# Optimization experiments

Hardware: AMD Instinct MI355X
Metric: run time of the kernel (lower is better)

## Reference

```python
import jax, jax.numpy as jnp
import numpy as np

CC = 0.25  # commitment cost
K1 = 4096
K2 = 4096
D1 = 64
D2 = 64

def conv1d(x, w, b, stride=1, pad=0):
    # x: [N,C,T], w: [O,I,K] (torch layout)
    y = jax.lax.conv_general_dilated(x, w, (stride,), [(pad, pad)],
                                     dimension_numbers=('NCH', 'OIH', 'NCH'))
    return y + b[None, :, None]

def convT1d(x, w, b, stride=2, pad=1):
    # torch ConvTranspose1d weight layout: [Cin, Cout, K]
    k = w.shape[-1]
    w2 = jnp.flip(w, -1).transpose(1, 0, 2)  # -> [Cout, Cin, K]
    y = jax.lax.conv_general_dilated(x, w2, (1,), [(k - 1 - pad, k - 1 - pad)],
                                     lhs_dilation=(stride,),
                                     dimension_numbers=('NCH', 'OIH', 'NCH'))
    return y + b[None, :, None]

def resblocks(x, w1, b1, w2, b2):
    # w1: [n, C, C, 3], w2: [n, C, C, 1]; n is small & fixed (2)
    for i in range(w1.shape[0]):
        h = conv1d(jax.nn.relu(x), w1[i], b1[i], 1, 1)
        h = conv1d(jax.nn.relu(h), w2[i], b2[i], 1, 0)
        x = x + h
    return x

def quantize(x, embed):
    # x: [B,D,T]; embed: [K,D]
    b, d, t = x.shape
    xf = x.transpose(0, 2, 1).reshape(-1, d)               # [N,D]
    dist = (xf * xf).sum(1, keepdims=True) - 2.0 * (xf @ embed.T) + (embed * embed).sum(1)
    idx = jnp.argmin(dist, axis=1)                          # [N]
    q = embed[idx]                                          # gather == onehot @ embed
    commit = CC * jnp.mean((jax.lax.stop_gradient(q) - xf) ** 2)
    q = xf + jax.lax.stop_gradient(q - xf)                  # straight-through
    q = q.reshape(b, t, d).transpose(0, 2, 1)
    K = embed.shape[0]
    avg = jnp.zeros(K, xf.dtype).at[idx].add(1.0) / xf.shape[0]
    perp = jnp.exp(-jnp.sum(avg * jnp.log(avg + 1e-10)))
    usage = jnp.sum(avg * jnp.log(avg * K + 1e-10))
    return q, commit, perp, usage

def setup_inputs() -> dict:
    key = jax.random.key(0)
    ks = iter(jax.random.split(key, 64))
    def p(*shape):
        return jax.random.normal(next(ks), shape, jnp.float32) * 0.05
    inp = {}
    inp['x'] = jax.random.normal(next(ks), (16, 1, 8192), jnp.float32)
    c1, c2, c3 = 128, 256, 384
    # Encoder
    inp['e_c1_w'] = p(c1, 1, 7);   inp['e_c1_b'] = p(c1)
    inp['e_r1_w1'] = p(2, c1, c1, 3); inp['e_r1_b1'] = p(2, c1)
    inp['e_r1_w2'] = p(2, c1, c1, 1); inp['e_r1_b2'] = p(2, c1)
    inp['e_c2_w'] = p(c2, c1, 5);  inp['e_c2_b'] = p(c2)
    inp['e_r2_w1'] = p(2, c2, c2, 3); inp['e_r2_b1'] = p(2, c2)
    inp['e_r2_w2'] = p(2, c2, c2, 1); inp['e_r2_b2'] = p(2, c2)
    inp['e_c3_w'] = p(c3, c2, 3);  inp['e_c3_b'] = p(c3)
    inp['e_r3_w1'] = p(2, c3, c3, 3); inp['e_r3_b1'] = p(2, c3)
    inp['e_r3_w2'] = p(2, c3, c3, 1); inp['e_r3_b2'] = p(2, c3)
    inp['e_pr_w'] = p(128, c3, 1); inp['e_pr_b'] = p(128)
    # Codebooks (torch.randn init)
    inp['emb1'] = jax.random.normal(next(ks), (K1, D1), jnp.float32)
    inp['emb2'] = jax.random.normal(next(ks), (K2, D2), jnp.float32)
    # Decoder
    inp['d_pr_w'] = p(c3, 128, 1); inp['d_pr_b'] = p(c3)
    inp['d_r1_w1'] = p(2, c3, c3, 3); inp['d_r1_b1'] = p(2, c3)
    inp['d_r1_w2'] = p(2, c3, c3, 1); inp['d_r1_b2'] = p(2, c3)
    inp['d_u1_w'] = p(c3, c2, 4);  inp['d_u1_b'] = p(c2)  # ConvTranspose: [Cin,Cout,K]
    inp['d_r2_w1'] = p(2, c2, c2, 3); inp['d_r2_b1'] = p(2, c2)
    inp['d_r2_w2'] = p(2, c2, c2, 1); inp['d_r2_b2'] = p(2, c2)
    inp['d_u2_w'] = p(c2, c1, 4);  inp['d_u2_b'] = p(c1)
    inp['d_r3_w1'] = p(2, c1, c1, 3); inp['d_r3_b1'] = p(2, c1)
    inp['d_r3_w2'] = p(2, c1, c1, 1); inp['d_r3_b2'] = p(2, c1)
    inp['d_u3_w'] = p(c1, c1, 4);  inp['d_u3_b'] = p(c1)
    inp['d_out_w'] = p(1, c1, 7);  inp['d_out_b'] = p(1)
    return inp

def reference(x, e_c1_w, e_c1_b, e_r1_w1, e_r1_b1, e_r1_w2, e_r1_b2,
              e_c2_w, e_c2_b, e_r2_w1, e_r2_b1, e_r2_w2, e_r2_b2,
              e_c3_w, e_c3_b, e_r3_w1, e_r3_b1, e_r3_w2, e_r3_b2,
              e_pr_w, e_pr_b, emb1, emb2,
              d_pr_w, d_pr_b, d_r1_w1, d_r1_b1, d_r1_w2, d_r1_b2,
              d_u1_w, d_u1_b, d_r2_w1, d_r2_b1, d_r2_w2, d_r2_b2,
              d_u2_w, d_u2_b, d_r3_w1, d_r3_b1, d_r3_w2, d_r3_b2,
              d_u3_w, d_u3_b, d_out_w, d_out_b):
    # Encoder
    z = conv1d(x, e_c1_w, e_c1_b, stride=2, pad=3)
    z = resblocks(z, e_r1_w1, e_r1_b1, e_r1_w2, e_r1_b2)
    z = conv1d(z, e_c2_w, e_c2_b, stride=2, pad=2)
    z = resblocks(z, e_r2_w1, e_r2_b1, e_r2_w2, e_r2_b2)
    z = conv1d(z, e_c3_w, e_c3_b, stride=2, pad=1)
    z = resblocks(z, e_r3_w1, e_r3_b1, e_r3_w2, e_r3_b2)
    z = conv1d(z, e_pr_w, e_pr_b)
    # Product VQ
    q1, c1l, p1, u1 = quantize(z[:, :D1], emb1)
    q2, c2l, p2, u2 = quantize(z[:, D1:], emb2)
    q = jnp.concatenate([q1, q2], axis=1)
    # Decoder
    h = conv1d(q, d_pr_w, d_pr_b)
    h = resblocks(h, d_r1_w1, d_r1_b1, d_r1_w2, d_r1_b2)
    h = convT1d(h, d_u1_w, d_u1_b)
    h = resblocks(h, d_r2_w1, d_r2_b1, d_r2_w2, d_r2_b2)
    h = convT1d(h, d_u2_w, d_u2_b)
    h = resblocks(h, d_r3_w1, d_r3_b1, d_r3_w2, d_r3_b2)
    h = convT1d(h, d_u3_w, d_u3_b)
    x_hat = conv1d(h, d_out_w, d_out_b, stride=1, pad=3)
    return (x_hat, c1l + c2l, u1 + u2, p1, p2)
```

## Files before the change

kernel.cpp:

```cpp
#include <hip/hip_runtime.h>
#include <math.h>

#define TPB 256
typedef __bf16 bf16x8 __attribute__((ext_vector_type(8)));
typedef float f32x4 __attribute__((ext_vector_type(4)));

static __device__ __forceinline__ float bf2f(unsigned short h) {
    union { unsigned int u; float f; } x; x.u = ((unsigned int)h) << 16; return x.f;
}
static __device__ __forceinline__ unsigned short f2bf(float f) {
    union { float f; unsigned int u; } x; x.f = f;
    unsigned int r = x.u + 0x7FFFu + ((x.u >> 16) & 1u);
    return (unsigned short)(r >> 16);
}
static __device__ __forceinline__ unsigned int relu_pk(unsigned int v) {
    unsigned int hi = (v & 0x80000000u) ? 0u : (v & 0xFFFF0000u);
    unsigned int lo = (v & 0x8000u) ? 0u : (v & 0xFFFFu);
    return hi | lo;
}
static __device__ __forceinline__ f32x4 MFMA(bf16x8 a, bf16x8 b, f32x4 c) {
    return __builtin_amdgcn_mfma_f32_16x16x32_bf16(a, b, c, 0, 0, 0);
}

template<int K, bool RELU>
__global__ __launch_bounds__(TPB) void conv1d_k(
    const float* __restrict__ x, const float* __restrict__ w,
    const float* __restrict__ bias, const float* __restrict__ res,
    float* __restrict__ y,
    int N, int Ci, int T, int Co, int To, int stride, int pad)
{
    int id = blockIdx.x * TPB + threadIdx.x;
    int total = N * Co * To;
    if (id >= total) return;
    int to = id % To;
    int co = (id / To) % Co;
    int n  = id / (To * Co);
    const float* xn = x + (size_t)n * Ci * T;
    const float* wc = w + (size_t)co * Ci * K;
    float acc = bias[co];
    int h0 = to * stride - pad;
    for (int ci = 0; ci < Ci; ++ci) {
        const float* xc = xn + (size_t)ci * T;
        const float* wk = wc + (size_t)ci * K;
        #pragma unroll
        for (int k = 0; k < K; ++k) {
            int pos = h0 + k;
            if (pos >= 0 && pos < T) {
                float v = xc[pos];
                if (RELU) v = fmaxf(v, 0.0f);
                acc = fmaf(v, wk[k], acc);
            }
        }
    }
    if (res) acc += res[id];
    y[id] = acc;
}

template<int K, int S, bool RELU, bool RES>
__global__ __launch_bounds__(TPB) void conv_tile_k(
    const float* __restrict__ x, const float* __restrict__ w,
    const float* __restrict__ bias, const float* __restrict__ res,
    float* __restrict__ y, int Ci, int Ti, int Co, int To)
{
    constexpr int CC    = 16;
    constexpr int TNEED = 127 * S + K;
    constexpr int RS    = ((TNEED + 3) & ~3) + 4;
    constexpr int NXV   = 7 * S + K;
    constexpr int NV4   = (NXV + 3) / 4;
    constexpr int WROW  = 68;
    __shared__ float xs[CC][RS];
    __shared__ float ws[CC * K * WROW];

    const int tid   = threadIdx.x;
    const int co_g  = tid & 15;
    const int t_g   = tid >> 4;
    const int tg8S  = t_g * 8 * S;
    const int co_g4 = co_g * 4;
    const int n     = blockIdx.z;
    const int co0   = blockIdx.y * 64;
    const int tb    = blockIdx.x * 128;
    const int t0in  = tb * S - K / 2;

    float4 b4 = *(const float4*)&bias[co0 + co_g4];
    float bi[4] = {b4.x, b4.y, b4.z, b4.w};
    float acc[4][8];
    #pragma unroll
    for (int i = 0; i < 4; ++i)
        #pragma unroll
        for (int j = 0; j < 8; ++j) acc[i][j] = bi[i];

    const int nchunk = Ci / CC;
    for (int ch = 0; ch < nchunk; ++ch) {
        const int ci0 = ch * CC;
        __syncthreads();
        for (int lin = tid; lin < CC * TNEED; lin += TPB) {
            int r = lin / TNEED, off = lin - r * TNEED;
            int t = t0in + off;
            float v = 0.f;
            if (t >= 0 && t < Ti) {
                v = x[((size_t)(n * Ci + ci0 + r)) * Ti + t];
                if (RELU) v = fmaxf(v, 0.f);
            }
            xs[r][off] = v;
        }
        for (int lin = tid; lin < 64 * CC * K; lin += TPB) {
            int co_l = lin / (CC * K), rem = lin - co_l * (CC * K);
            ws[rem * WROW + co_l] =
                w[(size_t)(co0 + co_l) * Ci * K + (size_t)ci0 * K + rem];
        }
        __syncthreads();
        for (int r = 0; r < CC; ++r) {
            float xv[NV4 * 4];
            #pragma unroll
            for (int q = 0; q < NV4; ++q)
                *(float4*)&xv[q * 4] = *(const float4*)&xs[r][tg8S + q * 4];
            #pragma unroll
            for (int k = 0; k < K; ++k) {
                float4 wv = *(const float4*)&ws[(r * K + k) * WROW + co_g4];
                float wa[4] = {wv.x, wv.y, wv.z, wv.w};
                #pragma unroll
                for (int i = 0; i < 4; ++i)
                    #pragma unroll
                    for (int j = 0; j < 8; ++j)
                        acc[i][j] = fmaf(wa[i], xv[j * S + k], acc[i][j]);
            }
        }
    }
    #pragma unroll
    for (int i = 0; i < 4; ++i) {
        size_t yb = ((size_t)(n * Co + co0 + co_g4 + i)) * To + tb + t_g * 8;
        float4 lo = make_float4(acc[i][0], acc[i][1], acc[i][2], acc[i][3]);
        float4 hi = make_float4(acc[i][4], acc[i][5], acc[i][6], acc[i][7]);
        if (RES) {
            float4 r0 = *(const float4*)&res[yb];
            float4 r1 = *(const float4*)&res[yb + 4];
            lo.x += r0.x; lo.y += r0.y; lo.z += r0.z; lo.w += r0.w;
            hi.x += r1.x; hi.y += r1.y; hi.z += r1.z; hi.w += r1.w;
        }
        *(float4*)&y[yb]     = lo;
        *(float4*)&y[yb + 4] = hi;
    }
}

template<int K, int TOFF, bool RELU, bool RES, int OSTR, int OOFF>
__global__ __launch_bounds__(TPB) void gconv_k(
    const unsigned short* __restrict__ x, const unsigned short* __restrict__ wp,
    const float* __restrict__ bias, const unsigned short* __restrict__ res,
    unsigned short* __restrict__ y, int Ci, int Tin, int Co, int Tout)
{
    constexpr int XR = 64 + K - 1;
    __shared__ unsigned short x_lds[XR * 40];
    __shared__ unsigned short w_lds[K * 64 * 40];
    const int tid = threadIdx.x;
    const int n = blockIdx.z, co0 = blockIdx.y * 64, P = blockIdx.x * 64;
    const int wid = tid >> 6, l = tid & 63;
    const int wm = wid >> 1, wn = wid & 1;
    const int lr = l & 15, kg = l >> 4;
    f32x4 acc[2][2] = {{{0.f,0.f,0.f,0.f},{0.f,0.f,0.f,0.f}},
                       {{0.f,0.f,0.f,0.f},{0.f,0.f,0.f,0.f}}};
    const int nch = Ci >> 5;
    for (int cc = 0; cc < nch; ++cc) {
        __syncthreads();
        for (int i = tid; i < XR * 4; i += TPB) {
            int r = i >> 2, c4 = i & 3;
            int gr = P + TOFF + r;
            uint4 v = make_uint4(0u, 0u, 0u, 0u);
            if (gr >= 0 && gr < Tin)
                v = *(const uint4*)(x + ((size_t)(n * Tin + gr) * Ci + cc * 32 + c4 * 8));
            if (RELU) { v.x = relu_pk(v.x); v.y = relu_pk(v.y);
                        v.z = relu_pk(v.z); v.w = relu_pk(v.w); }
            *(uint4*)&x_lds[r * 40 + c4 * 8] = v;
        }
        for (int i = tid; i < K * 64 * 4; i += TPB) {
            int r2 = i >> 2, c4 = i & 3;
            *(uint4*)&w_lds[r2 * 40 + c4 * 8] =
                *(const uint4*)(wp + ((size_t)((r2 >> 6) * Co + co0 + (r2 & 63)) * Ci
                                      + cc * 32 + c4 * 8));
        }
        __syncthreads();
        #pragma unroll
        for (int kk = 0; kk < K; ++kk) {
            bf16x8 av0 = *(const bf16x8*)&x_lds[(wm * 32 +      lr + kk) * 40 + kg * 8];
            bf16x8 av1 = *(const bf16x8*)&x_lds[(wm * 32 + 16 + lr + kk) * 40 + kg * 8];
            bf16x8 bv0 = *(const bf16x8*)&w_lds[(kk * 64 + wn * 32 +      lr) * 40 + kg * 8];
            bf16x8 bv1 = *(const bf16x8*)&w_lds[(kk * 64 + wn * 32 + 16 + lr) * 40 + kg * 8];
            acc[0][0] = MFMA(av0, bv0, acc[0][0]);
            acc[0][1] = MFMA(av0, bv1, acc[0][1]);
            acc[1][0] = MFMA(av1, bv0, acc[1][0]);
            acc[1][1] = MFMA(av1, bv1, acc[1][1]);
        }
    }
    float bb[2] = { bias[co0 + wn * 32 + lr], bias[co0 + wn * 32 + 16 + lr] };
    #pragma unroll
    for (int mf = 0; mf < 2; ++mf)
        #pragma unroll
        for (int nf = 0; nf < 2; ++nf) {
            int co = co0 + wn * 32 + nf * 16 + lr;
            #pragma unroll
            for (int r = 0; r < 4; ++r) {
                int m = wm * 32 + mf * 16 + kg * 4 + r;
                int orow = (P + m) * OSTR + OOFF;
                float v = acc[mf][nf][r] + bb[nf];
                size_t oidx = ((size_t)n * Tout + orow) * Co + co;
                if (RES) v += bf2f(res[oidx]);
                y[oidx] = f2bf(v);
            }
        }
}

__global__ __launch_bounds__(TPB) void prep_conv_k(
    const float* __restrict__ w, unsigned short* __restrict__ out, int Co, int Ci, int K)
{
    int id = blockIdx.x * TPB + threadIdx.x;
    if (id >= K * Co * Ci) return;
    int ci = id % Ci, co = (id / Ci) % Co, k = id / (Ci * Co);
    out[id] = f2bf(w[((size_t)co * Ci + ci) * K + k]);
}
__global__ __launch_bounds__(TPB) void prep_convt_k(
    const float* __restrict__ w, unsigned short* __restrict__ oute,
    unsigned short* __restrict__ outo, int Co, int Ci)
{
    int id = blockIdx.x * TPB + threadIdx.x;
    if (id >= 2 * Co * Ci) return;
    int ci = id % Ci, co = (id / Ci) % Co, kp = id / (Ci * Co);
    const float* src = w + ((size_t)ci * Co + co) * 4;
    oute[id] = f2bf(src[3 - 2 * kp]);
    outo[id] = f2bf(src[2 - 2 * kp]);
}

__global__ __launch_bounds__(TPB) void dout_cl_k(
    const unsigned short* __restrict__ x, const float* __restrict__ w,
    const float* __restrict__ b, float* __restrict__ y)
{
    __shared__ unsigned short xs[262 * 40];
    const int tid = threadIdx.x;
    const int tb = blockIdx.x * 256;
    const int n = blockIdx.y;
    float acc = b[0];
    for (int cc = 0; cc < 4; ++cc) {
        __syncthreads();
        for (int i = tid; i < 262 * 4; i += TPB) {
            int r = i >> 2, c4 = i & 3;
            int gr = tb - 3 + r;
            uint4 v = make_uint4(0u, 0u, 0u, 0u);
            if (gr >= 0 && gr < 8192)
                v = *(const uint4*)(x + ((size_t)(n * 8192 + gr) * 128 + cc * 32 + c4 * 8));
            *(uint4*)&xs[r * 40 + c4 * 8] = v;
        }
        __syncthreads();
        #pragma unroll
        for (int k = 0; k < 7; ++k) {
            const unsigned short* row = &xs[(tid + k) * 40];
            #pragma unroll
            for (int e = 0; e < 32; ++e)
                acc = fmaf(bf2f(row[e]), w[(cc * 32 + e) * 7 + k], acc);
        }
    }
    y[(size_t)n * 8192 + tb + tid] = acc;
}

#define NVEC 16384
#define KC   4096
#define DD   64
#define NCH  16

__global__ __launch_bounds__(TPB) void vq_norms_k(
    const float* __restrict__ emb1, const float* __restrict__ emb2,
    float* __restrict__ enorm)
{
    int id = blockIdx.x * TPB + threadIdx.x;
    if (id >= 2 * KC) return;
    const float* e = (id < KC) ? (emb1 + (size_t)id * DD) : (emb2 + (size_t)(id - KC) * DD);
    float s = 0.f;
    #pragma unroll
    for (int d = 0; d < DD; ++d) s = fmaf(e[d], e[d], s);
    enorm[id] = s;
}

__global__ __launch_bounds__(TPB) void vq_partial_k(
    const float* __restrict__ z,
    const float* __restrict__ emb1, const float* __restrict__ emb2,
    const float* __restrict__ enorm,
    float* __restrict__ pmin, int* __restrict__ pidx)
{
    int v  = blockIdx.x * TPB + threadIdx.x;
    int ch = blockIdx.y;
    int cb = blockIdx.z;
    const float* emb = cb ? emb2 : emb1;
    const float* en  = enorm + cb * KC;
    int b = v >> 10, t = v & 1023;
    const float* zp = z + ((size_t)b * 128 + cb * 64) * 1024 + t;
    float xv[DD];
    #pragma unroll
    for (int d = 0; d < DD; ++d) xv[d] = zp[(size_t)d * 1024];

    float best = 1e30f; int bi = 0;
    const int c0 = ch * (KC / NCH);
    for (int c = c0; c < c0 + KC / NCH; ++c) {
        const float* e = emb + (size_t)c * DD;
        float p0 = 0.f, p1 = 0.f, p2 = 0.f, p3 = 0.f;
        #pragma unroll
        for (int d = 0; d < DD; d += 4) {
            p0 = fmaf(xv[d],     e[d],     p0);
            p1 = fmaf(xv[d + 1], e[d + 1], p1);
            p2 = fmaf(xv[d + 2], e[d + 2], p2);
            p3 = fmaf(xv[d + 3], e[d + 3], p3);
        }
        float s = en[c] - 2.0f * ((p0 + p1) + (p2 + p3));
        if (s < best) { best = s; bi = c; }
    }
    float xn = 0.f;
    #pragma unroll
    for (int d = 0; d < DD; ++d) xn = fmaf(xv[d], xv[d], xn);
    pmin[((size_t)cb * NCH + ch) * NVEC + v] = best + xn;
    pidx[((size_t)cb * NCH + ch) * NVEC + v] = bi;
}

__global__ __launch_bounds__(TPB) void vq_finalize_k(
    const float* __restrict__ pmin, const int* __restrict__ pidx,
    int* __restrict__ idxf, float* __restrict__ cnt, float* __restrict__ csum)
{
    int gid = blockIdx.x * TPB + threadIdx.x;
    int cb  = gid >> 14;
    int v   = gid & (NVEC - 1);
    float best = pmin[((size_t)cb * NCH + 0) * NVEC + v];
    int   bi   = pidx[((size_t)cb * NCH + 0) * NVEC + v];
    #pragma unroll
    for (int ch = 1; ch < NCH; ++ch) {
        float m  = pmin[((size_t)cb * NCH + ch) * NVEC + v];
        int   ix = pidx[((size_t)cb * NCH + ch) * NVEC + v];
        if (m < best) { best = m; bi = ix; }
    }
    idxf[cb * NVEC + v] = bi;
    atomicAdd(&cnt[cb * KC + bi], 1.0f);
    float s = best;
    #pragma unroll
    for (int off = 32; off; off >>= 1) s += __shfl_down(s, off, 64);
    __shared__ float wsum[4];
    int wid = threadIdx.x >> 6;
    if ((threadIdx.x & 63) == 0) wsum[wid] = s;
    __syncthreads();
    if (threadIdx.x == 0)
        atomicAdd(&csum[cb], wsum[0] + wsum[1] + wsum[2] + wsum[3]);
}

__global__ __launch_bounds__(TPB) void vq_gather_cl_k(
    const int* __restrict__ idxf,
    const float* __restrict__ emb1, const float* __restrict__ emb2,
    unsigned short* __restrict__ q)
{
    int id = blockIdx.x * TPB + threadIdx.x;
    int c = id & 127;
    int t = (id >> 7) & 1023;
    int n = id >> 17;
    int cb = c >> 6, d = c & 63;
    int idx = idxf[cb * NVEC + n * 1024 + t];
    const float* emb = cb ? emb2 : emb1;
    q[id] = f2bf(emb[(size_t)idx * DD + d]);
}

__global__ __launch_bounds__(TPB) void vq_stats_k(
    const float* __restrict__ cnt, const float* __restrict__ csum,
    float* __restrict__ out)
{
    float h0 = 0.f, h1 = 0.f, u0 = 0.f, u1 = 0.f;
    for (int i = threadIdx.x; i < KC; i += TPB) {
        float a0 = cnt[i]      * (1.0f / NVEC);
        float a1 = cnt[KC + i] * (1.0f / NVEC);
        h0 -= a0 * logf(a0 + 1e-10f);
        h1 -= a1 * logf(a1 + 1e-10f);
        u0 += a0 * logf(a0 * (float)KC + 1e-10f);
        u1 += a1 * logf(a1 * (float)KC + 1e-10f);
    }
    #pragma unroll
    for (int off = 32; off; off >>= 1) {
        h0 += __shfl_down(h0, off, 64);
        h1 += __shfl_down(h1, off, 64);
        u0 += __shfl_down(u0, off, 64);
        u1 += __shfl_down(u1, off, 64);
    }
    __shared__ float red[4][4];
    int wid = threadIdx.x >> 6;
    if ((threadIdx.x & 63) == 0) {
        red[wid][0] = h0; red[wid][1] = h1; red[wid][2] = u0; red[wid][3] = u1;
    }
    __syncthreads();
    if (threadIdx.x == 0) {
        h0 = red[0][0] + red[1][0] + red[2][0] + red[3][0];
        h1 = red[0][1] + red[1][1] + red[2][1] + red[3][1];
        u0 = red[0][2] + red[1][2] + red[2][2] + red[3][2];
        u1 = red[0][3] + red[1][3] + red[2][3] + red[3][3];
        out[0] = 0.25f * (csum[0] + csum[1]) * (1.0f / ((float)NVEC * (float)DD));
        out[1] = u0 + u1;
        out[2] = expf(h0);
        out[3] = expf(h1);
    }
}

template<int K, int S, bool RELU, bool RES>
static void launch_conv(hipStream_t st, const float* x, const float* w, const float* b,
                        const float* res, float* y, int Ci, int Ti, int Co, int To)
{
    dim3 g(To / 128, Co / 64, 16);
    conv_tile_k<K, S, RELU, RES><<<g, TPB, 0, st>>>(x, w, b, res, y, Ci, Ti, Co, To);
}

static void resblocks_t(hipStream_t st, float** cur, float** f1, float** f2,
                        const float* w1, const float* b1, const float* w2, const float* b2,
                        int C, int T)
{
    for (int i = 0; i < 2; ++i) {
        launch_conv<3, 1, true, false>(st, *cur, w1 + (size_t)i * C * C * 3, b1 + i * C,
                                       nullptr, *f1, C, T, C, T);
        launch_conv<1, 1, true, true>(st, *f1, w2 + (size_t)i * C * C, b2 + i * C,
                                      *cur, *f2, C, T, C, T);
        float* t = *cur; *cur = *f2; *f2 = t;
    }
}

template<int K, int TOFF, bool RELU, bool RES, int OSTR, int OOFF>
static void gconv(hipStream_t st, const unsigned short* x, const unsigned short* wp,
                  const float* b, const unsigned short* res, unsigned short* y,
                  int Ci, int Tin, int Co, int Tout)
{
    dim3 g(Tin / 64, Co / 64, 16);
    gconv_k<K, TOFF, RELU, RES, OSTR, OOFF><<<g, TPB, 0, st>>>(x, wp, b, res, y,
                                                               Ci, Tin, Co, Tout);
}

static void dresblock(hipStream_t st, unsigned short* cur, unsigned short* o1,
                      unsigned short* o2, const unsigned short* wpc1,
                      const unsigned short* wpc2, const float* b1, const float* b2,
                      int C, int T)
{
    size_t wc1 = (size_t)3 * C * C, wc2 = (size_t)C * C;
    gconv<3, -1, true, false, 1, 0>(st, cur, wpc1, b1, nullptr, o1, C, T, C, T);
    gconv<1,  0, true, true,  1, 0>(st, o1, wpc2, b2, cur, o2, C, T, C, T);
    gconv<3, -1, true, false, 1, 0>(st, o2, wpc1 + wc1, b1 + C, nullptr, o1, C, T, C, T);
    gconv<1,  0, true, true,  1, 0>(st, o1, wpc2 + wc2, b2 + C, o2, cur, C, T, C, T);
}

static void prep_conv(hipStream_t st, const float* w, unsigned short* out,
                      int Co, int Ci, int K)
{
    int n = K * Co * Ci;
    prep_conv_k<<<(n + TPB - 1) / TPB, TPB, 0, st>>>(w, out, Co, Ci, K);
}
static void prep_convt(hipStream_t st, const float* w, unsigned short* oe,
                       unsigned short* oo, int Co, int Ci)
{
    int n = 2 * Co * Ci;
    prep_convt_k<<<(n + TPB - 1) / TPB, TPB, 0, st>>>(w, oe, oo, Co, Ci);
}

extern "C" void kernel_launch(void* const* d_in, const int* in_sizes, int n_in,
                              void* d_out, int out_size, void* d_ws, size_t ws_size,
                              hipStream_t stream)
{
    const float* x       = (const float*)d_in[0];
    const float* e_c1_w  = (const float*)d_in[1];
    const float* e_c1_b  = (const float*)d_in[2];
    const float* e_r1_w1 = (const float*)d_in[3];
    const float* e_r1_b1 = (const float*)d_in[4];
    const float* e_r1_w2 = (const float*)d_in[5];
    const float* e_r1_b2 = (const float*)d_in[6];
    const float* e_c2_w  = (const float*)d_in[7];
    const float* e_c2_b  = (const float*)d_in[8];
    const float* e_r2_w1 = (const float*)d_in[9];
    const float* e_r2_b1 = (const float*)d_in[10];
    const float* e_r2_w2 = (const float*)d_in[11];
    const float* e_r2_b2 = (const float*)d_in[12];
    const float* e_c3_w  = (const float*)d_in[13];
    const float* e_c3_b  = (const float*)d_in[14];
    const float* e_r3_w1 = (const float*)d_in[15];
    const float* e_r3_b1 = (const float*)d_in[16];
    const float* e_r3_w2 = (const float*)d_in[17];
    const float* e_r3_b2 = (const float*)d_in[18];
    const float* e_pr_w  = (const float*)d_in[19];
    const float* e_pr_b  = (const float*)d_in[20];
    const float* emb1    = (const float*)d_in[21];
    const float* emb2    = (const float*)d_in[22];
    const float* d_pr_w  = (const float*)d_in[23];
    const float* d_pr_b  = (const float*)d_in[24];
    const float* d_r1_w1 = (const float*)d_in[25];
    const float* d_r1_b1 = (const float*)d_in[26];
    const float* d_r1_w2 = (const float*)d_in[27];
    const float* d_r1_b2 = (const float*)d_in[28];
    const float* d_u1_w  = (const float*)d_in[29];
    const float* d_u1_b  = (const float*)d_in[30];
    const float* d_r2_w1 = (const float*)d_in[31];
    const float* d_r2_b1 = (const float*)d_in[32];
    const float* d_r2_w2 = (const float*)d_in[33];
    const float* d_r2_b2 = (const float*)d_in[34];
    const float* d_u2_w  = (const float*)d_in[35];
    const float* d_u2_b  = (const float*)d_in[36];
    const float* d_r3_w1 = (const float*)d_in[37];
    const float* d_r3_b1 = (const float*)d_in[38];
    const float* d_r3_w2 = (const float*)d_in[39];
    const float* d_r3_b2 = (const float*)d_in[40];
    const float* d_u3_w  = (const float*)d_in[41];
    const float* d_u3_b  = (const float*)d_in[42];
    const float* d_outw  = (const float*)d_in[43];
    const float* d_outb  = (const float*)d_in[44];

    const size_t BUF = 16777216;
    float* W0   = (float*)d_ws;
    float* W1   = W0 + BUF;
    float* W2   = W1 + BUF;
    float* pmin = W2 + BUF;
    int*   pidx = (int*)(pmin + 524288);
    int*   idxf = pidx + 524288;
    float* enorm= (float*)(idxf + 32768);
    float* cnt  = enorm + 8192;
    float* csum = cnt + 8192;
    unsigned short* wp = (unsigned short*)(csum + 4);

    unsigned short* wp_dpr  = wp;
    unsigned short* wp_r1c1 = wp_dpr  + 49152;
    unsigned short* wp_r1c2 = wp_r1c1 + 884736;
    unsigned short* wp_u1e  = wp_r1c2 + 294912;
    unsigned short* wp_u1o  = wp_u1e  + 196608;
    unsigned short* wp_r2c1 = wp_u1o  + 196608;
    unsigned short* wp_r2c2 = wp_r2c1 + 393216;
    unsigned short* wp_u2e  = wp_r2c2 + 131072;
    unsigned short* wp_u2o  = wp_u2e  + 65536;
    unsigned short* wp_r3c1 = wp_u2o  + 65536;
    unsigned short* wp_r3c2 = wp_r3c1 + 98304;
    unsigned short* wp_u3e  = wp_r3c2 + 32768;
    unsigned short* wp_u3o  = wp_u3e  + 32768;

    unsigned short* bfA = (unsigned short*)W0;
    unsigned short* bfB = bfA + BUF;
    unsigned short* bfC = (unsigned short*)W2;

    float *A = W0, *B = W1, *C = W2, *t_;
    hipStream_t st = stream;

    prep_conv(st, d_pr_w, wp_dpr, 384, 128, 1);
    prep_conv(st, d_r1_w1,                      wp_r1c1,          384, 384, 3);
    prep_conv(st, d_r1_w1 + (size_t)384*384*3,  wp_r1c1 + 442368, 384, 384, 3);
    prep_conv(st, d_r1_w2,                      wp_r1c2,          384, 384, 1);
    prep_conv(st, d_r1_w2 + (size_t)384*384,    wp_r1c2 + 147456, 384, 384, 1);
    prep_convt(st, d_u1_w, wp_u1e, wp_u1o, 256, 384);
    prep_conv(st, d_r2_w1,                      wp_r2c1,          256, 256, 3);
    prep_conv(st, d_r2_w1 + (size_t)256*256*3,  wp_r2c1 + 196608, 256, 256, 3);
    prep_conv(st, d_r2_w2,                      wp_r2c2,          256, 256, 1);
    prep_conv(st, d_r2_w2 + (size_t)256*256,    wp_r2c2 + 65536,  256, 256, 1);
    prep_convt(st, d_u2_w, wp_u2e, wp_u2o, 128, 256);
    prep_conv(st, d_r3_w1,                      wp_r3c1,          128, 128, 3);
    prep_conv(st, d_r3_w1 + (size_t)128*128*3,  wp_r3c1 + 49152,  128, 128, 3);
    prep_conv(st, d_r3_w2,                      wp_r3c2,          128, 128, 1);
    prep_conv(st, d_r3_w2 + (size_t)128*128,    wp_r3c2 + 16384,  128, 128, 1);
    prep_convt(st, d_u3_w, wp_u3e, wp_u3o, 128, 128);

    {
        int total = 16 * 128 * 4096;
        conv1d_k<7, false><<<(total + TPB - 1) / TPB, TPB, 0, st>>>(
            x, e_c1_w, e_c1_b, nullptr, A, 16, 1, 8192, 128, 4096, 2, 3);
    }
    resblocks_t(st, &A, &B, &C, e_r1_w1, e_r1_b1, e_r1_w2, e_r1_b2, 128, 4096);
    launch_conv<5, 2, false, false>(st, A, e_c2_w, e_c2_b, nullptr, B, 128, 4096, 256, 2048);
    t_ = A; A = B; B = t_;
    resblocks_t(st, &A, &B, &C, e_r2_w1, e_r2_b1, e_r2_w2, e_r2_b2, 256, 2048);
    launch_conv<3, 2, false, false>(st, A, e_c3_w, e_c3_b, nullptr, B, 256, 2048, 384, 1024);
    t_ = A; A = B; B = t_;
    resblocks_t(st, &A, &B, &C, e_r3_w1, e_r3_b1, e_r3_w2, e_r3_b2, 384, 1024);
    launch_conv<1, 1, false, false>(st, A, e_pr_w, e_pr_b, nullptr, B, 384, 1024, 128, 1024);
    t_ = A; A = B; B = t_;

    hipMemsetAsync(cnt, 0, (8192 + 4) * sizeof(float), st);
    vq_norms_k<<<(2 * KC + TPB - 1) / TPB, TPB, 0, st>>>(emb1, emb2, enorm);
    dim3 pg(NVEC / TPB, NCH, 2);
    vq_partial_k<<<pg, TPB, 0, st>>>(A, emb1, emb2, enorm, pmin, pidx);
    vq_finalize_k<<<2 * NVEC / TPB, TPB, 0, st>>>(pmin, pidx, idxf, cnt, csum);
    vq_gather_cl_k<<<16 * 1024 * 128 / TPB, TPB, 0, st>>>(idxf, emb1, emb2, bfA);

    gconv<1, 0, false, false, 1, 0>(st, bfA, wp_dpr, d_pr_b, nullptr, bfB,
                                    128, 1024, 384, 1024);
    dresblock(st, bfB, bfA, bfC, wp_r1c1, wp_r1c2, d_r1_b1, d_r1_b2, 384, 1024);
    gconv<2, -1, false, false, 2, 0>(st, bfB, wp_u1e, d_u1_b, nullptr, bfA,
                                     384, 1024, 256, 2048);
    gconv<2,  0, false, false, 2, 1>(st, bfB, wp_u1o, d_u1_b, nullptr, bfA,
                                     384, 1024, 256, 2048);
    dresblock(st, bfA, bfB, bfC, wp_r2c1, wp_r2c2, d_r2_b1, d_r2_b2, 256, 2048);
    gconv<2, -1, false, false, 2, 0>(st, bfA, wp_u2e, d_u2_b, nullptr, bfB,
                                     256, 2048, 128, 4096);
    gconv<2,  0, false, false, 2, 1>(st, bfA, wp_u2o, d_u2_b, nullptr, bfB,
                                     256, 2048, 128, 4096);
    dresblock(st, bfB, bfA, bfC, wp_r3c1, wp_r3c2, d_r3_b1, d_r3_b2, 128, 4096);
    gconv<2, -1, false, false, 2, 0>(st, bfB, wp_u3e, d_u3_b, nullptr, bfA,
                                     128, 4096, 128, 8192);
    gconv<2,  0, false, false, 2, 1>(st, bfB, wp_u3o, d_u3_b, nullptr, bfA,
                                     128, 4096, 128, 8192);
    {
        dim3 g(8192 / 256, 16);
        dout_cl_k<<<g, TPB, 0, st>>>(bfA, d_outw, d_outb, (float*)d_out);
    }

    vq_stats_k<<<1, TPB, 0, st>>>(cnt, csum, (float*)d_out + 131072);
}
```

Baseline: 3.154 ms.

## Fuse even/odd transposed-conv phases and register-block VQ search over two vectors

Adds a single transposed-conv kernel that computes the even and odd output phases together. The input tile is loaded into LDS once and shared by both MFMA accumulator sets, replacing the two separate launches that each reloaded it. The VQ distance kernel now handles two vectors per thread with float4-vectorised codebook loads, so each codebook row fetched serves two vectors. It also sets an occupancy hint of 3 via launch_bounds. The costs are higher register pressure in both kernels and larger LDS use in the fused conv.

```diff
diff --git a/kernel.cpp b/kernel.cpp
--- a/kernel.cpp
+++ b/kernel.cpp
@@ -208,6 +208,77 @@
         }
 }
 
+__global__ __launch_bounds__(TPB) void gconvt_k(
+    const unsigned short* __restrict__ x, const unsigned short* __restrict__ wpe,
+    const unsigned short* __restrict__ wpo, const float* __restrict__ bias,
+    unsigned short* __restrict__ y, int Ci, int Tin, int Co)
+{
+    __shared__ unsigned short x_lds[66 * 40];
+    __shared__ unsigned short we_lds[2 * 64 * 40];
+    __shared__ unsigned short wo_lds[2 * 64 * 40];
+    const int tid = threadIdx.x;
+    const int n = blockIdx.z, co0 = blockIdx.y * 64, P = blockIdx.x * 64;
+    const int wid = tid >> 6, l = tid & 63;
+    const int wm = wid >> 1, wn = wid & 1;
+    const int lr = l & 15, kg = l >> 4;
+    f32x4 accE[2][2] = {{{0.f,0.f,0.f,0.f},{0.f,0.f,0.f,0.f}},
+                        {{0.f,0.f,0.f,0.f},{0.f,0.f,0.f,0.f}}};
+    f32x4 accO[2][2] = {{{0.f,0.f,0.f,0.f},{0.f,0.f,0.f,0.f}},
+                        {{0.f,0.f,0.f,0.f},{0.f,0.f,0.f,0.f}}};
+    const int nch = Ci >> 5;
+    for (int cc = 0; cc < nch; ++cc) {
+        __syncthreads();
+        for (int i = tid; i < 66 * 4; i += TPB) {
+            int r = i >> 2, c4 = i & 3;
+            int gr = P - 1 + r;
+            uint4 v = make_uint4(0u, 0u, 0u, 0u);
+            if (gr >= 0 && gr < Tin)
+                v = *(const uint4*)(x + ((size_t)(n * Tin + gr) * Ci + cc * 32 + c4 * 8));
+            *(uint4*)&x_lds[r * 40 + c4 * 8] = v;
+        }
+        for (int i = tid; i < 2 * 64 * 4; i += TPB) {
+            int r2 = i >> 2, c4 = i & 3;
+            size_t off = (size_t)((r2 >> 6) * Co + co0 + (r2 & 63)) * Ci + cc * 32 + c4 * 8;
+            *(uint4*)&we_lds[r2 * 40 + c4 * 8] = *(const uint4*)(wpe + off);
+            *(uint4*)&wo_lds[r2 * 40 + c4 * 8] = *(const uint4*)(wpo + off);
+        }
+        __syncthreads();
+        #pragma unroll
+        for (int kk = 0; kk < 2; ++kk) {
+            bf16x8 aE0 = *(const bf16x8*)&x_lds[(wm * 32 +      lr + kk) * 40 + kg * 8];
+            bf16x8 aE1 = *(const bf16x8*)&x_lds[(wm * 32 + 16 + lr + kk) * 40 + kg * 8];
+            bf16x8 bE0 = *(const bf16x8*)&we_lds[(kk * 64 + wn * 32 +      lr) * 40 + kg * 8];
+            bf16x8 bE1 = *(const bf16x8*)&we_lds[(kk * 64 + wn * 32 + 16 + lr) * 40 + kg * 8];
+            accE[0][0] = MFMA(aE0, bE0, accE[0][0]);
+            accE[0][1] = MFMA(aE0, bE1, accE[0][1]);
+            accE[1][0] = MFMA(aE1, bE0, accE[1][0]);
+            accE[1][1] = MFMA(aE1, bE1, accE[1][1]);
+            bf16x8 aO0 = *(const bf16x8*)&x_lds[(wm * 32 +      lr + kk + 1) * 40 + kg * 8];
+            bf16x8 aO1 = *(const bf16x8*)&x_lds[(wm * 32 + 16 + lr + kk + 1) * 40 + kg * 8];
+            bf16x8 bO0 = *(const bf16x8*)&wo_lds[(kk * 64 + wn * 32 +      lr) * 40 + kg * 8];
+            bf16x8 bO1 = *(const bf16x8*)&wo_lds[(kk * 64 + wn * 32 + 16 + lr) * 40 + kg * 8];
+            accO[0][0] = MFMA(aO0, bO0, accO[0][0]);
+            accO[0][1] = MFMA(aO0, bO1, accO[0][1]);
+            accO[1][0] = MFMA(aO1, bO0, accO[1][0]);
+            accO[1][1] = MFMA(aO1, bO1, accO[1][1]);
+        }
+    }
+    float bb[2] = { bias[co0 + wn * 32 + lr], bias[co0 + wn * 32 + 16 + lr] };
+    #pragma unroll
+    for (int mf = 0; mf < 2; ++mf)
+        #pragma unroll
+        for (int nf = 0; nf < 2; ++nf) {
+            int co = co0 + wn * 32 + nf * 16 + lr;
+            #pragma unroll
+            for (int r = 0; r < 4; ++r) {
+                int m = wm * 32 + mf * 16 + kg * 4 + r;
+                size_t oe = ((size_t)n * (2 * Tin) + (size_t)(P + m) * 2) * Co + co;
+                y[oe]      = f2bf(accE[mf][nf][r] + bb[nf]);
+                y[oe + Co] = f2bf(accO[mf][nf][r] + bb[nf]);
+            }
+        }
+}
+
 __global__ __launch_bounds__(TPB) void prep_conv_k(
     const float* __restrict__ w, unsigned short* __restrict__ out, int Co, int Ci, int K)
 {
@@ -277,43 +348,69 @@
     enorm[id] = s;
 }
 
-__global__ __launch_bounds__(TPB) void vq_partial_k(
+__global__ __launch_bounds__(TPB, 3) void vq_partial_k(
     const float* __restrict__ z,
     const float* __restrict__ emb1, const float* __restrict__ emb2,
     const float* __restrict__ enorm,
     float* __restrict__ pmin, int* __restrict__ pidx)
 {
-    int v  = blockIdx.x * TPB + threadIdx.x;
-    int ch = blockIdx.y;
-    int cb = blockIdx.z;
+    const int v0 = blockIdx.x * (TPB * 2) + threadIdx.x;
+    const int v1 = v0 + TPB;
+    const int ch = blockIdx.y, cb = blockIdx.z;
     const float* emb = cb ? emb2 : emb1;
     const float* en  = enorm + cb * KC;
-    int b = v >> 10, t = v & 1023;
-    const float* zp = z + ((size_t)b * 128 + cb * 64) * 1024 + t;
-    float xv[DD];
-    #pragma unroll
-    for (int d = 0; d < DD; ++d) xv[d] = zp[(size_t)d * 1024];
-
-    float best = 1e30f; int bi = 0;
+
+    f32x4 xa[16], xb[16];
+    {
+        int b = v0 >> 10, t = v0 & 1023;
+        const float* zp = z + ((size_t)b * 128 + cb * 64) * 1024 + t;
+        #pragma unroll
+        for (int i = 0; i < 16; ++i) {
+            xa[i][0] = zp[(size_t)(4 * i + 0) * 1024];
+            xa[i][1] = zp[(size_t)(4 * i + 1) * 1024];
+            xa[i][2] = zp[(size_t)(4 * i + 2) * 1024];
+            xa[i][3] = zp[(size_t)(4 * i + 3) * 1024];
+        }
+    }
+    {
+        int b = v1 >> 10, t = v1 & 1023;
+        const float* zp = z + ((size_t)b * 128 + cb * 64) * 1024 + t;
+        #pragma unroll
+        for (int i = 0; i < 16; ++i) {
+            xb[i][0] = zp[(size_t)(4 * i + 0) * 1024];
+            xb[i][1] = zp[(size_t)(4 * i + 1) * 1024];
+            xb[i][2] = zp[(size_t)(4 * i + 2) * 1024];
+            xb[i][3] = zp[(size_t)(4 * i + 3) * 1024];
+        }
+    }
+
+    float best0 = 1e30f, best1 = 1e30f; int bi0 = 0, bi1 = 0;
     const int c0 = ch * (KC / NCH);
     for (int c = c0; c < c0 + KC / NCH; ++c) {
-        const float* e = emb + (size_t)c * DD;
-        float p0 = 0.f, p1 = 0.f, p2 = 0.f, p3 = 0.f;
-        #pragma unroll
-        for (int d = 0; d < DD; d += 4) {
-            p0 = fmaf(xv[d],     e[d],     p0);
-            p1 = fmaf(xv[d + 1], e[d + 1], p1);
-            p2 = fmaf(xv[d + 2], e[d + 2], p2);
-            p3 = fmaf(xv[d + 3], e[d + 3], p3);
-        }
-        float s = en[c] - 2.0f * ((p0 + p1) + (p2 + p3));
-        if (s < best) { best = s; bi = c; }
-    }
-    float xn = 0.f;
-    #pragma unroll
-    for (int d = 0; d < DD; ++d) xn = fmaf(xv[d], xv[d], xn);
-    pmin[((size_t)cb * NCH + ch) * NVEC + v] = best + xn;
-    pidx[((size_t)cb * NCH + ch) * NVEC + v] = bi;
+        const f32x4* e4 = (const f32x4*)(emb + (size_t)c * DD);
+        f32x4 pa = {0.f, 0.f, 0.f, 0.f}, pb = {0.f, 0.f, 0.f, 0.f};
+        #pragma unroll
+        for (int i = 0; i < 16; ++i) {
+            f32x4 ev = e4[i];
+            pa += xa[i] * ev;
+            pb += xb[i] * ev;
+        }
+        float enc = en[c];
+        float sa = enc - 2.0f * ((pa[0] + pa[1]) + (pa[2] + pa[3]));
+        float sb = enc - 2.0f * ((pb[0] + pb[1]) + (pb[2] + pb[3]));
+        if (sa < best0) { best0 = sa; bi0 = c; }
+        if (sb < best1) { best1 = sb; bi1 = c; }
+    }
+    f32x4 na = {0.f,0.f,0.f,0.f}, nb = {0.f,0.f,0.f,0.f};
+    #pragma unroll
+    for (int i = 0; i < 16; ++i) { na += xa[i] * xa[i]; nb += xb[i] * xb[i]; }
+    float xn0 = (na[0] + na[1]) + (na[2] + na[3]);
+    float xn1 = (nb[0] + nb[1]) + (nb[2] + nb[3]);
+    size_t base = ((size_t)cb * NCH + ch) * NVEC;
+    pmin[base + v0] = best0 + xn0;
+    pidx[base + v0] = bi0;
+    pmin[base + v1] = best1 + xn1;
+    pidx[base + v1] = bi1;
 }
 
 __global__ __launch_bounds__(TPB) void vq_finalize_k(
@@ -426,6 +523,14 @@
     dim3 g(Tin / 64, Co / 64, 16);
     gconv_k<K, TOFF, RELU, RES, OSTR, OOFF><<<g, TPB, 0, st>>>(x, wp, b, res, y,
                                                                Ci, Tin, Co, Tout);
+}
+
+static void gconvt2(hipStream_t st, const unsigned short* x, const unsigned short* we,
+                    const unsigned short* wo, const float* b, unsigned short* y,
+                    int Ci, int Tin, int Co)
+{
+    dim3 g(Tin / 64, Co / 64, 16);
+    gconvt_k<<<g, TPB, 0, st>>>(x, we, wo, b, y, Ci, Tin, Co);
 }
 
 static void dresblock(hipStream_t st, unsigned short* cur, unsigned short* o1,
@@ -570,7 +675,7 @@
 
     hipMemsetAsync(cnt, 0, (8192 + 4) * sizeof(float), st);
     vq_norms_k<<<(2 * KC + TPB - 1) / TPB, TPB, 0, st>>>(emb1, emb2, enorm);
-    dim3 pg(NVEC / TPB, NCH, 2);
+    dim3 pg(NVEC / (TPB * 2), NCH, 2);
     vq_partial_k<<<pg, TPB, 0, st>>>(A, emb1, emb2, enorm, pmin, pidx);
     vq_finalize_k<<<2 * NVEC / TPB, TPB, 0, st>>>(pmin, pidx, idxf, cnt, csum);
     vq_gather_cl_k<<<16 * 1024 * 128 / TPB, TPB, 0, st>>>(idxf, emb1, emb2, bfA);
@@ -578,20 +683,11 @@
     gconv<1, 0, false, false, 1, 0>(st, bfA, wp_dpr, d_pr_b, nullptr, bfB,
                                     128, 1024, 384, 1024);
     dresblock(st, bfB, bfA, bfC, wp_r1c1, wp_r1c2, d_r1_b1, d_r1_b2, 384, 1024);
-    gconv<2, -1, false, false, 2, 0>(st, bfB, wp_u1e, d_u1_b, nullptr, bfA,
-                                     384, 1024, 256, 2048);
-    gconv<2,  0, false, false, 2, 1>(st, bfB, wp_u1o, d_u1_b, nullptr, bfA,
-                                     384, 1024, 256, 2048);
+    gconvt2(st, bfB, wp_u1e, wp_u1o, d_u1_b, bfA, 384, 1024, 256);
     dresblock(st, bfA, bfB, bfC, wp_r2c1, wp_r2c2, d_r2_b1, d_r2_b2, 256, 2048);
-    gconv<2, -1, false, false, 2, 0>(st, bfA, wp_u2e, d_u2_b, nullptr, bfB,
-                                     256, 2048, 128, 4096);
-    gconv<2,  0, false, false, 2, 1>(st, bfA, wp_u2o, d_u2_b, nullptr, bfB,
-                                     256, 2048, 128, 4096);
+    gconvt2(st, bfA, wp_u2e, wp_u2o, d_u2_b, bfB, 256, 2048, 128);
     dresblock(st, bfB, bfA, bfC, wp_r3c1, wp_r3c2, d_r3_b1, d_r3_b2, 128, 4096);
-    gconv<2, -1, false, false, 2, 0>(st, bfB, wp_u3e, d_u3_b, nullptr, bfA,
-                                     128, 4096, 128, 8192);
-    gconv<2,  0, false, false, 2, 1>(st, bfB, wp_u3o, d_u3_b, nullptr, bfA,
-                                     128, 4096, 128, 8192);
+    gconvt2(st, bfB, wp_u3e, wp_u3o, d_u3_b, bfA, 128, 4096, 128);
     {
         dim3 g(8192 / 256, 16);
         dout_cl_k<<<g, TPB, 0, st>>>(bfA, d_outw, d_outb, (float*)d_out);
```

New measurement: 3.082 ms. -2.3%, faster.
